# Kernel tuning notes

Measured on AMD Instinct MI355X. Metric: run time of the kernel, lower is better.

The kernel has to match this reference:

```python
import jax, jax.numpy as jnp
import numpy as np

B, N, D, C, Q = 8, 2048, 512, 4096, 4


def l2norm(x):
    return x / jnp.maximum(jnp.linalg.norm(x, axis=-1, keepdims=True), 1e-12)


def rotate_to(src, tgt):
    # rotation-trick transform: rotate src onto tgt, rotation detached
    sg = jax.lax.stop_gradient
    ns = jnp.linalg.norm(src, axis=-1, keepdims=True)
    nt = jnp.linalg.norm(tgt, axis=-1, keepdims=True)
    u = src / ns
    q = tgt / nt
    w = sg(l2norm(u + q))  # Householder bisector, detached
    e = src
    r = (e
         - 2.0 * jnp.sum(e * w, axis=-1, keepdims=True) * w
         + 2.0 * jnp.sum(e * sg(u), axis=-1, keepdims=True) * q)
    return r * sg(nt / ns)


def setup_inputs() -> dict:
    key = jax.random.key(0)
    k1, k2, k3 = jax.random.split(key, 3)
    x = jax.random.normal(k1, (B, N, D), jnp.float32)
    codebooks = jax.random.normal(k2, (Q, C, D), jnp.float32) * D ** -0.5
    weights = jax.random.normal(k3, (Q, D, D), jnp.float32) * D ** -0.5
    return {"x": x, "codebooks": codebooks, "weights": weights}


def reference(x, codebooks, weights):
    sg = jax.lax.stop_gradient
    num_q = codebooks.shape[0]
    residual = x
    quantized_out = jnp.zeros_like(x)
    all_idx, all_loss = [], []
    for i in range(num_q):
        implicit_cb = codebooks[i] @ weights[i].T  # Linear(dim,dim,bias=False)
        cb_n = l2norm(implicit_cb)                 # [C, D]
        x_n = l2norm(residual)                     # [B, N, D]
        # argmax of cosine similarity (no_grad in torch)
        sim = jnp.einsum('bnd,cd->bnc', sg(x_n), sg(cb_n))
        idx = jnp.argmax(sim, axis=-1)             # [B, N]
        quant = cb_n[idx]                          # [B, N, D]
        commit = (jnp.mean((sg(x_n) - quant) ** 2)
                  + 0.25 * jnp.mean((x_n - sg(quant)) ** 2))
        quant = rotate_to(x_n, quant)
        residual = residual - sg(quant)
        quantized_out = quantized_out + quant
        all_idx.append(idx)
        all_loss.append(commit)
    return quantized_out, jnp.stack(all_idx, axis=-1), jnp.stack(all_loss, axis=-1)
```

## Files before the change

kernel.cpp:

```cpp
#include <hip/hip_runtime.h>
#include <math.h>

#define RR 16384
#define DD 512
#define CC 4096
#define QQ 4
#define QOUT_SZ (RR*DD)
#define IDX_OFF QOUT_SZ
#define LOSS_OFF (QOUT_SZ + RR*QQ)
#define LOSS_COEF (1.25f / 8388608.0f)
#define NBLK_FIN (RR/4)

#define WS_RESID 0
#define WS_CBN   (RR*DD)
#define WS_RNRM  (WS_CBN + CC*DD)
#define WS_PV    (WS_RNRM + RR)
#define WS_PI    (WS_PV + RR*32*4)
#define WS_F16   (WS_PI + RR*32*4 + 4)
#define F16_A 0
#define F16_B (RR*DD)

typedef _Float16 f16x8 __attribute__((ext_vector_type(8)));
typedef short bf16x8 __attribute__((ext_vector_type(8)));
typedef float f32x4 __attribute__((ext_vector_type(4)));

__device__ __forceinline__ float waveSum(float v) {
#pragma unroll
    for (int m = 1; m < 64; m <<= 1) v += __shfl_xor(v, m, 64);
    return v;
}

template <int N>
__device__ __forceinline__ void waveSumN(float* v) {
#pragma unroll
    for (int m = 1; m < 64; m <<= 1) {
#pragma unroll
        for (int j = 0; j < N; ++j) v[j] += __shfl_xor(v[j], m, 64);
    }
}

__device__ __forceinline__ unsigned packKey(float v, int c) {
    unsigned u = __float_as_uint(v);
    u ^= (unsigned)((int)u >> 31) | 0x80000000u;
    return (u & 0xFFFFF000u) | (unsigned)(4095 - c);
}

__device__ __forceinline__ void ceDesc(unsigned &a, unsigned &b) {
    unsigned mn = a > b ? b : a;
    a = a > b ? a : b;
    b = mn;
}

__device__ __forceinline__ void merge4(unsigned k[4],
                                       unsigned b0, unsigned b1,
                                       unsigned b2, unsigned b3) {
    k[0] = k[0] > b3 ? k[0] : b3;
    k[1] = k[1] > b2 ? k[1] : b2;
    k[2] = k[2] > b1 ? k[2] : b1;
    k[3] = k[3] > b0 ? k[3] : b0;
    ceDesc(k[0], k[2]); ceDesc(k[1], k[3]);
    ceDesc(k[0], k[1]); ceDesc(k[2], k[3]);
}

__device__ __forceinline__ void merge4Shfl(unsigned k[4], int m) {
    unsigned b0 = __shfl_xor(k[0], m, 64);
    unsigned b1 = __shfl_xor(k[1], m, 64);
    unsigned b2 = __shfl_xor(k[2], m, 64);
    unsigned b3 = __shfl_xor(k[3], m, 64);
    merge4(k, b0, b1, b2, b3);
}

__device__ __forceinline__ unsigned bf16rne(float x) {
    unsigned u = __float_as_uint(x);
    return (u + 0x7FFFu + ((u >> 16) & 1u)) >> 16;
}

__global__ void initK(const float* __restrict__ x, float* __restrict__ resid) {
    int i = blockIdx.x * blockDim.x + threadIdx.x;
    int stride = gridDim.x * blockDim.x;
    for (; i < QOUT_SZ; i += stride) resid[i] = x[i];
}

__global__ void cvtSplitK(const float* __restrict__ src, short* __restrict__ hi,
                          short* __restrict__ lo, int n) {
    int i = (blockIdx.x * blockDim.x + threadIdx.x) * 4;
    int stride = gridDim.x * blockDim.x * 4;
    for (; i < n; i += stride) {
        float4 v = *(const float4*)&src[i];
        float vv[4] = {v.x, v.y, v.z, v.w};
        short hh[4], ll[4];
#pragma unroll
        for (int j = 0; j < 4; ++j) {
            unsigned hb = bf16rne(vv[j]);
            float hf = __uint_as_float(hb << 16);
            hh[j] = (short)hb;
            ll[j] = (short)bf16rne(vv[j] - hf);
        }
        *(short4*)&hi[i] = make_short4(hh[0], hh[1], hh[2], hh[3]);
        *(short4*)&lo[i] = make_short4(ll[0], ll[1], ll[2], ll[3]);
    }
}

__global__ __launch_bounds__(256)
void gemmCbMfmaK(const short* __restrict__ AHi, const short* __restrict__ ALo,
                 const short* __restrict__ BHi, const short* __restrict__ BLo,
                 float* __restrict__ out) {
    __shared__ short AH[64 * 64], AL[64 * 64];
    __shared__ short BH[64 * 64], BL[64 * 64];
    int t = threadIdx.x, w = t >> 6, lane = t & 63;
    int cBase = blockIdx.x * 64, dBase = blockIdx.y * 64;
    int mbase = (w & 1) * 32, nbase = (w >> 1) * 32;
    int l15 = lane & 15, quad = lane >> 4;

    f32x4 acc[2][2];
#pragma unroll
    for (int i = 0; i < 2; ++i)
#pragma unroll
        for (int j = 0; j < 2; ++j) acc[i][j] = (f32x4){0.f, 0.f, 0.f, 0.f};

    int rsub = lane >> 3;
    int swz = (lane & 7) ^ rsub;

    for (int k0 = 0; k0 < DD; k0 += 64) {
        __syncthreads();
#pragma unroll
        for (int j = 0; j < 2; ++j) {
            int r0 = j * 32 + 8 * w;
            __builtin_amdgcn_global_load_lds(
                (const __attribute__((address_space(1))) void*)&AHi[(size_t)(cBase + r0 + rsub) * DD + k0 + swz * 8],
                (__attribute__((address_space(3))) void*)&AH[r0 * 64], 16, 0, 0);
            __builtin_amdgcn_global_load_lds(
                (const __attribute__((address_space(1))) void*)&ALo[(size_t)(cBase + r0 + rsub) * DD + k0 + swz * 8],
                (__attribute__((address_space(3))) void*)&AL[r0 * 64], 16, 0, 0);
            __builtin_amdgcn_global_load_lds(
                (const __attribute__((address_space(1))) void*)&BHi[(size_t)(dBase + r0 + rsub) * DD + k0 + swz * 8],
                (__attribute__((address_space(3))) void*)&BH[r0 * 64], 16, 0, 0);
            __builtin_amdgcn_global_load_lds(
                (const __attribute__((address_space(1))) void*)&BLo[(size_t)(dBase + r0 + rsub) * DD + k0 + swz * 8],
                (__attribute__((address_space(3))) void*)&BL[r0 * 64], 16, 0, 0);
        }
        __syncthreads();
#pragma unroll
        for (int kh = 0; kh < 2; ++kh) {
            int chunk = (kh * 4 + quad) ^ (l15 & 7);
            bf16x8 ah[2], al[2], bh[2], bl[2];
#pragma unroll
            for (int tm = 0; tm < 2; ++tm) {
                ah[tm] = *(const bf16x8*)&AH[(mbase + tm * 16 + l15) * 64 + chunk * 8];
                al[tm] = *(const bf16x8*)&AL[(mbase + tm * 16 + l15) * 64 + chunk * 8];
            }
#pragma unroll
            for (int tn = 0; tn < 2; ++tn) {
                bh[tn] = *(const bf16x8*)&BH[(nbase + tn * 16 + l15) * 64 + chunk * 8];
                bl[tn] = *(const bf16x8*)&BL[(nbase + tn * 16 + l15) * 64 + chunk * 8];
            }
#pragma unroll
            for (int tn = 0; tn < 2; ++tn)
#pragma unroll
                for (int tm = 0; tm < 2; ++tm) {
                    acc[tm][tn] = __builtin_amdgcn_mfma_f32_16x16x32_bf16(
                        ah[tm], bh[tn], acc[tm][tn], 0, 0, 0);
                    acc[tm][tn] = __builtin_amdgcn_mfma_f32_16x16x32_bf16(
                        ah[tm], bl[tn], acc[tm][tn], 0, 0, 0);
                    acc[tm][tn] = __builtin_amdgcn_mfma_f32_16x16x32_bf16(
                        al[tm], bh[tn], acc[tm][tn], 0, 0, 0);
                }
        }
    }

#pragma unroll
    for (int tm = 0; tm < 2; ++tm)
#pragma unroll
        for (int tn = 0; tn < 2; ++tn)
#pragma unroll
            for (int r = 0; r < 4; ++r) {
                int row = cBase + mbase + tm * 16 + quad * 4 + r;
                int col = dBase + nbase + tn * 16 + l15;
                out[(size_t)row * DD + col] = acc[tm][tn][r];
            }
}

__global__ void rowNormCvtK(float* __restrict__ buf, _Float16* __restrict__ bf16) {
    int wave = threadIdx.x >> 6, lane = threadIdx.x & 63;
    int row = blockIdx.x * 4 + wave;
    float* p = buf + (size_t)row * DD;
    float4 v0 = *(float4*)&p[lane * 8];
    float4 v1 = *(float4*)&p[lane * 8 + 4];
    float ss = v0.x*v0.x + v0.y*v0.y + v0.z*v0.z + v0.w*v0.w
             + v1.x*v1.x + v1.y*v1.y + v1.z*v1.z + v1.w*v1.w;
    ss = waveSum(ss);
    float nrm = fmaxf(sqrtf(ss), 1e-12f);
    float vals[8] = {v0.x/nrm, v0.y/nrm, v0.z/nrm, v0.w/nrm,
                     v1.x/nrm, v1.y/nrm, v1.z/nrm, v1.w/nrm};
    *(float4*)&p[lane * 8]     = make_float4(vals[0], vals[1], vals[2], vals[3]);
    *(float4*)&p[lane * 8 + 4] = make_float4(vals[4], vals[5], vals[6], vals[7]);
    f16x8 hv;
#pragma unroll
    for (int j = 0; j < 8; ++j) hv[j] = (_Float16)vals[j];
    *(f16x8*)&bf16[(size_t)row * DD + lane * 8] = hv;
}

__global__ void residCvtK(const float* __restrict__ resid,
                          float* __restrict__ rnrm, _Float16* __restrict__ af16) {
    int wave = threadIdx.x >> 6, lane = threadIdx.x & 63;
    int row = blockIdx.x * 4 + wave;
    const float* p = resid + (size_t)row * DD;
    float4 v0 = *(const float4*)&p[lane * 8];
    float4 v1 = *(const float4*)&p[lane * 8 + 4];
    float vals[8] = {v0.x, v0.y, v0.z, v0.w, v1.x, v1.y, v1.z, v1.w};
    float ss = 0.f;
#pragma unroll
    for (int j = 0; j < 8; ++j) ss += vals[j] * vals[j];
    ss = waveSum(ss);
    if (lane == 0) rnrm[row] = fmaxf(sqrtf(ss), 1e-12f);
    f16x8 hv;
#pragma unroll
    for (int j = 0; j < 8; ++j) hv[j] = (_Float16)vals[j];
    *(f16x8*)&af16[(size_t)row * DD + lane * 8] = hv;
}

__global__ __launch_bounds__(512)
void simMfmaK(
    const _Float16* __restrict__ Af16, const _Float16* __restrict__ Bf16,
    unsigned* __restrict__ pk) {
    __shared__ _Float16 Alds[2][128 * 64];
    __shared__ _Float16 Blds[2][128 * 64];
    int t = threadIdx.x, w = t >> 6, lane = t & 63;
    int rowBase = blockIdx.x * 128;
    int cBase = blockIdx.y * 128;
    int mbase = (w & 3) * 32, nbase = (w >> 2) * 64;
    int l15 = lane & 15, quad = lane >> 4;

    f32x4 acc[2][4];
#pragma unroll
    for (int i = 0; i < 2; ++i)
#pragma unroll
        for (int j = 0; j < 4; ++j) acc[i][j] = (f32x4){0.f, 0.f, 0.f, 0.f};

    int rsub = lane >> 3;
    int swz = (lane & 7) ^ rsub;

#define SIM_STAGE(b, tt)                                                          \
    {                                                                             \
        int k0s = (tt) * 64;                                                      \
        _Pragma("unroll")                                                         \
        for (int j = 0; j < 2; ++j) {                                             \
            int rA = rowBase + j * 64 + 8 * w + rsub;                             \
            int rB = cBase + j * 64 + 8 * w + rsub;                               \
            __builtin_amdgcn_global_load_lds(                                     \
                (const __attribute__((address_space(1))) void*)&Af16[(size_t)rA * DD + k0s + swz * 8], \
                (__attribute__((address_space(3))) void*)&Alds[b][(j * 64 + 8 * w) * 64], 16, 0, 0);   \
            __builtin_amdgcn_global_load_lds(                                     \
                (const __attribute__((address_space(1))) void*)&Bf16[(size_t)rB * DD + k0s + swz * 8], \
                (__attribute__((address_space(3))) void*)&Blds[b][(j * 64 + 8 * w) * 64], 16, 0, 0);   \
        }                                                                         \
    }

    SIM_STAGE(0, 0);

#pragma unroll
    for (int tt = 0; tt < 8; ++tt) {
        int buf = tt & 1;
        if (tt < 7) {
            SIM_STAGE(buf ^ 1, tt + 1);
            asm volatile("s_waitcnt vmcnt(4)" ::: "memory");
        } else {
            asm volatile("s_waitcnt vmcnt(0)" ::: "memory");
        }
        __builtin_amdgcn_s_barrier();
        __builtin_amdgcn_sched_barrier(0);
#pragma unroll
        for (int kh = 0; kh < 2; ++kh) {
            int chunk = (kh * 4 + quad) ^ (l15 & 7);
            f16x8 af[2];
#pragma unroll
            for (int tm = 0; tm < 2; ++tm)
                af[tm] = *(const f16x8*)&Alds[buf][(mbase + tm * 16 + l15) * 64 + chunk * 8];
#pragma unroll
            for (int tn = 0; tn < 4; ++tn) {
                f16x8 bf = *(const f16x8*)&Blds[buf][(nbase + tn * 16 + l15) * 64 + chunk * 8];
#pragma unroll
                for (int tm = 0; tm < 2; ++tm)
                    acc[tm][tn] = __builtin_amdgcn_mfma_f32_16x16x32_f16(
                        af[tm], bf, acc[tm][tn], 0, 0, 0);
            }
        }
        __builtin_amdgcn_sched_barrier(0);
        asm volatile("" ::: "memory");
        __builtin_amdgcn_s_barrier();
    }
#undef SIM_STAGE

    int gkey = (cBase >> 6) + (w >> 2);
#pragma unroll
    for (int tm = 0; tm < 2; ++tm) {
#pragma unroll
        for (int r = 0; r < 4; ++r) {
            unsigned t0 = packKey(acc[tm][0][r], cBase + nbase + 0 * 16 + l15);
            unsigned t1 = packKey(acc[tm][1][r], cBase + nbase + 1 * 16 + l15);
            unsigned t2 = packKey(acc[tm][2][r], cBase + nbase + 2 * 16 + l15);
            unsigned t3 = packKey(acc[tm][3][r], cBase + nbase + 3 * 16 + l15);
            ceDesc(t0, t1); ceDesc(t2, t3);
            unsigned k0 = t0 > t2 ? t0 : t2;
            unsigned mn = t0 > t2 ? t2 : t0;
            unsigned mx = t1 > t3 ? t1 : t3;
            unsigned k1 = mn > mx ? mn : mx;
#pragma unroll
            for (int m = 1; m < 16; m <<= 1) {
                unsigned b0 = __shfl_xor(k0, m, 64);
                unsigned b1 = __shfl_xor(k1, m, 64);
                unsigned m0 = k0 > b0 ? k0 : b0;
                unsigned n0 = k0 > b0 ? b0 : k0;
                unsigned m1 = k1 > b1 ? k1 : b1;
                k0 = m0;
                k1 = n0 > m1 ? n0 : m1;
            }
            if (l15 == 0) {
                int rowg = rowBase + mbase + tm * 16 + quad * 4 + r;
                *(uint2*)&pk[(size_t)rowg * 128 + gkey * 2] = make_uint2(k0, k1);
            }
        }
    }
}

__global__ void finalizeK(float* __restrict__ resid,
                          float* __restrict__ rnrm,
                          const float* __restrict__ cbn,
                          const unsigned* __restrict__ pk,
                          float* __restrict__ dout,
                          float* __restrict__ lossPart,
                          _Float16* __restrict__ af16, int q) {
    __shared__ float sL[4];
    int wave = threadIdx.x >> 6, lane = threadIdx.x & 63;
    int row = blockIdx.x * 4 + wave;
    float* xr = resid + (size_t)row * DD;
    float nrm = rnrm[row];
    float4 a0 = *(float4*)&xr[lane * 8];
    float4 a1 = *(float4*)&xr[lane * 8 + 4];
    float orig[8] = {a0.x,a0.y,a0.z,a0.w,a1.x,a1.y,a1.z,a1.w};
    float x[8];
#pragma unroll
    for (int j = 0; j < 8; ++j) x[j] = orig[j] / nrm;

    uint2 kp = *(const uint2*)&pk[(size_t)row * 128 + lane * 2];
    unsigned k[4] = {kp.x, kp.y, 0u, 0u};
#pragma unroll
    for (int m = 1; m < 64; m <<= 1) merge4Shfl(k, m);
    int cand[4];
#pragma unroll
    for (int j = 0; j < 4; ++j)
        cand[j] = 4095 - (int)(__shfl(k[j], 0, 64) & 0xFFFu);

    float cv[4][8];
#pragma unroll
    for (int j = 0; j < 4; ++j) {
        const float* cbj = cbn + (size_t)cand[j] * DD;
        float4 c0 = *(const float4*)&cbj[lane * 8];
        float4 c1 = *(const float4*)&cbj[lane * 8 + 4];
        cv[j][0]=c0.x; cv[j][1]=c0.y; cv[j][2]=c0.z; cv[j][3]=c0.w;
        cv[j][4]=c1.x; cv[j][5]=c1.y; cv[j][6]=c1.z; cv[j][7]=c1.w;
    }
    float s[4];
#pragma unroll
    for (int j = 0; j < 4; ++j) {
        float acc = 0.f;
#pragma unroll
        for (int e = 0; e < 8; ++e) acc += x[e] * cv[j][e];
        s[j] = acc;
    }
    waveSumN<4>(s);
    float sBest = -3e38f; int idx = 0x7fffffff, sel = 0;
#pragma unroll
    for (int j = 0; j < 4; ++j) {
        if (s[j] > sBest || (s[j] == sBest && cand[j] < idx)) {
            sBest = s[j]; idx = cand[j]; sel = j;
        }
    }

    float qv[8];
#pragma unroll
    for (int e = 0; e < 8; ++e)
        qv[e] = sel == 0 ? cv[0][e] : sel == 1 ? cv[1][e]
              : sel == 2 ? cv[2][e] : cv[3][e];

    float red3[3] = {0.f, 0.f, 0.f};
#pragma unroll
    for (int j = 0; j < 8; ++j) {
        red3[0] += x[j] * x[j];
        red3[1] += qv[j] * qv[j];
        float d = x[j] - qv[j];
        red3[2] += d * d;
    }
    waveSumN<3>(red3);
    float ns = sqrtf(red3[0]), nt = sqrtf(red3[1]), lrow = red3[2];

    float u[8], qn[8], wv[8];
    float nw2 = 0.f;
#pragma unroll
    for (int j = 0; j < 8; ++j) {
        u[j] = x[j] / ns;
        qn[j] = qv[j] / nt;
        wv[j] = u[j] + qn[j];
        nw2 += wv[j] * wv[j];
    }
    nw2 = waveSum(nw2);
    float nw = fmaxf(sqrtf(nw2), 1e-12f);
    float red2[2] = {0.f, 0.f};
#pragma unroll
    for (int j = 0; j < 8; ++j) {
        wv[j] = wv[j] / nw;
        red2[0] += x[j] * wv[j];
        red2[1] += x[j] * u[j];
    }
    waveSumN<2>(red2);
    float dew = red2[0], deu = red2[1];
    float scale = nt / ns;

    float r[8], nres[8];
    float ss = 0.f;
#pragma unroll
    for (int j = 0; j < 8; ++j) {
        r[j] = (x[j] - 2.0f * dew * wv[j] + 2.0f * deu * qn[j]) * scale;
        nres[j] = orig[j] - r[j];
        ss += nres[j] * nres[j];
    }

    *(float4*)&xr[lane * 8]     = make_float4(nres[0], nres[1], nres[2], nres[3]);
    *(float4*)&xr[lane * 8 + 4] = make_float4(nres[4], nres[5], nres[6], nres[7]);
    ss = waveSum(ss);
    if (lane == 0) rnrm[row] = fmaxf(sqrtf(ss), 1e-12f);
    f16x8 hv;
#pragma unroll
    for (int j = 0; j < 8; ++j) hv[j] = (_Float16)nres[j];
    *(f16x8*)&af16[(size_t)row * DD + lane * 8] = hv;

    if (lane == 0) {
        dout[IDX_OFF + row * 4 + q] = (float)idx;
        sL[wave] = lrow;
    }
    __syncthreads();
    if (threadIdx.x == 0) {
        lossPart[(size_t)q * NBLK_FIN + blockIdx.x] =
            (sL[0] + sL[1] + sL[2] + sL[3]) * LOSS_COEF;
    }
}

__global__ void qoutK(const float* __restrict__ x, const float* __restrict__ resid,
                      float* __restrict__ dout) {
    int i = blockIdx.x * blockDim.x + threadIdx.x;
    int stride = gridDim.x * blockDim.x;
    for (; i < QOUT_SZ; i += stride) dout[i] = x[i] - resid[i];
}

__global__ void lossWriteK(const float* __restrict__ lossPart,
                           float* __restrict__ dout) {
    int q = threadIdx.x >> 6, lane = threadIdx.x & 63;
    float s = 0.f;
    for (int i = lane; i < NBLK_FIN; i += 64)
        s += lossPart[(size_t)q * NBLK_FIN + i];
    s = waveSum(s);
    if (lane == 0) dout[LOSS_OFF + q] = s;
}

extern "C" void kernel_launch(void* const* d_in, const int* in_sizes, int n_in,
                              void* d_out, int out_size, void* d_ws, size_t ws_size,
                              hipStream_t stream) {
    const float* x = (const float*)d_in[0];
    const float* codebooks = (const float*)d_in[1];
    const float* weights = (const float*)d_in[2];
    float* dout = (float*)d_out;
    float* w = (float*)d_ws;

    float* resid = w + WS_RESID;
    float* cbn   = w + WS_CBN;
    float* rnrm  = w + WS_RNRM;
    unsigned* pk = (unsigned*)(w + WS_PV);
    float* lossPart = w + WS_PI;
    _Float16* f16base = (_Float16*)(w + WS_F16);
    _Float16* Af16 = f16base + F16_A;
    _Float16* Bf16 = f16base + F16_B;
    short* cbHi = (short*)(w + WS_PV);
    short* cbLo = cbHi + (size_t)CC * DD;
    short* wHi  = (short*)(w + WS_PI + 32768);
    short* wLo  = wHi + (size_t)DD * DD;

    initK<<<2048, 256, 0, stream>>>(x, resid);
    residCvtK<<<RR / 4, 256, 0, stream>>>(resid, rnrm, Af16);

    for (int q = 0; q < QQ; ++q) {
        cvtSplitK<<<512, 256, 0, stream>>>(codebooks + (size_t)q * CC * DD,
                                           cbHi, cbLo, CC * DD);
        cvtSplitK<<<128, 256, 0, stream>>>(weights + (size_t)q * DD * DD,
                                           wHi, wLo, DD * DD);
        gemmCbMfmaK<<<dim3(CC / 64, DD / 64), 256, 0, stream>>>(
            cbHi, cbLo, wHi, wLo, cbn);
        rowNormCvtK<<<CC / 4, 256, 0, stream>>>(cbn, Bf16);
        simMfmaK<<<dim3(RR / 128, CC / 128), 512, 0, stream>>>(Af16, Bf16, pk);
        finalizeK<<<RR / 4, 256, 0, stream>>>(resid, rnrm, cbn, pk,
                                              dout, lossPart, Af16, q);
    }
    qoutK<<<2048, 256, 0, stream>>>(x, resid, dout);
    lossWriteK<<<1, 256, 0, stream>>>(lossPart, dout);
}
```

Baseline: 773.7 us.

## Collapse rotation trick to codebook vector and use a single barrier per k-step

The finalize kernel relies on both inputs to the rotation being unit vectors, so the rotated result is exactly the selected normalized codeword. It drops the Householder reductions and the extra wave sums, and computes the commit loss as 2 - 2·cos. Candidate rescoring now uses the unnormalized residual, since a positive scale does not change the argmax. In the similarity GEMM, the wait and barrier move to the end of each k-step, so each iteration does one prefetch, its MFMAs, and one sync. This trades the old partial vmcnt overlap for fewer barriers. The algebraic shortcut may differ from the reference by floating-point rounding.

```diff
diff --git a/kernel.cpp b/kernel.cpp
--- a/kernel.cpp
+++ b/kernel.cpp
@@ -257,18 +257,14 @@
     }
 
     SIM_STAGE(0, 0);
+    asm volatile("s_waitcnt vmcnt(0)" ::: "memory");
+    __builtin_amdgcn_s_barrier();
+    __builtin_amdgcn_sched_barrier(0);
 
 #pragma unroll
     for (int tt = 0; tt < 8; ++tt) {
         int buf = tt & 1;
-        if (tt < 7) {
-            SIM_STAGE(buf ^ 1, tt + 1);
-            asm volatile("s_waitcnt vmcnt(4)" ::: "memory");
-        } else {
-            asm volatile("s_waitcnt vmcnt(0)" ::: "memory");
-        }
-        __builtin_amdgcn_s_barrier();
-        __builtin_amdgcn_sched_barrier(0);
+        if (tt < 7) SIM_STAGE(buf ^ 1, tt + 1);
 #pragma unroll
         for (int kh = 0; kh < 2; ++kh) {
             int chunk = (kh * 4 + quad) ^ (l15 & 7);
@@ -285,9 +281,12 @@
                         af[tm], bf, acc[tm][tn], 0, 0, 0);
             }
         }
-        __builtin_amdgcn_sched_barrier(0);
-        asm volatile("" ::: "memory");
-        __builtin_amdgcn_s_barrier();
+        if (tt < 7) {
+            __builtin_amdgcn_sched_barrier(0);
+            asm volatile("s_waitcnt vmcnt(0)" ::: "memory");
+            __builtin_amdgcn_s_barrier();
+            __builtin_amdgcn_sched_barrier(0);
+        }
     }
 #undef SIM_STAGE
 
@@ -338,9 +337,6 @@
     float4 a0 = *(float4*)&xr[lane * 8];
     float4 a1 = *(float4*)&xr[lane * 8 + 4];
     float orig[8] = {a0.x,a0.y,a0.z,a0.w,a1.x,a1.y,a1.z,a1.w};
-    float x[8];
-#pragma unroll
-    for (int j = 0; j < 8; ++j) x[j] = orig[j] / nrm;
 
     uint2 kp = *(const uint2*)&pk[(size_t)row * 128 + lane * 2];
     unsigned k[4] = {kp.x, kp.y, 0u, 0u};
@@ -365,7 +361,7 @@
     for (int j = 0; j < 4; ++j) {
         float acc = 0.f;
 #pragma unroll
-        for (int e = 0; e < 8; ++e) acc += x[e] * cv[j][e];
+        for (int e = 0; e < 8; ++e) acc += orig[e] * cv[j][e];
         s[j] = acc;
     }
     waveSumN<4>(s);
@@ -383,48 +379,15 @@
         qv[e] = sel == 0 ? cv[0][e] : sel == 1 ? cv[1][e]
               : sel == 2 ? cv[2][e] : cv[3][e];
 
-    float red3[3] = {0.f, 0.f, 0.f};
+    float lrow = 2.0f - 2.0f * (sBest / nrm);
+
+    float nres[8];
+    float ss = 0.f;
 #pragma unroll
     for (int j = 0; j < 8; ++j) {
-        red3[0] += x[j] * x[j];
-        red3[1] += qv[j] * qv[j];
-        float d = x[j] - qv[j];
-        red3[2] += d * d;
-    }
-    waveSumN<3>(red3);
-    float ns = sqrtf(red3[0]), nt = sqrtf(red3[1]), lrow = red3[2];
-
-    float u[8], qn[8], wv[8];
-    float nw2 = 0.f;
-#pragma unroll
-    for (int j = 0; j < 8; ++j) {
-        u[j] = x[j] / ns;
-        qn[j] = qv[j] / nt;
-        wv[j] = u[j] + qn[j];
-        nw2 += wv[j] * wv[j];
-    }
-    nw2 = waveSum(nw2);
-    float nw = fmaxf(sqrtf(nw2), 1e-12f);
-    float red2[2] = {0.f, 0.f};
-#pragma unroll
-    for (int j = 0; j < 8; ++j) {
-        wv[j] = wv[j] / nw;
-        red2[0] += x[j] * wv[j];
-        red2[1] += x[j] * u[j];
-    }
-    waveSumN<2>(red2);
-    float dew = red2[0], deu = red2[1];
-    float scale = nt / ns;
-
-    float r[8], nres[8];
-    float ss = 0.f;
-#pragma unroll
-    for (int j = 0; j < 8; ++j) {
-        r[j] = (x[j] - 2.0f * dew * wv[j] + 2.0f * deu * qn[j]) * scale;
-        nres[j] = orig[j] - r[j];
+        nres[j] = orig[j] - qv[j];
         ss += nres[j] * nres[j];
     }
-
     *(float4*)&xr[lane * 8]     = make_float4(nres[0], nres[1], nres[2], nres[3]);
     *(float4*)&xr[lane * 8 + 4] = make_float4(nres[4], nres[5], nres[6], nres[7]);
     ss = waveSum(ss);
```

Measured after the change: 752.5 us. 2.7% less time.
